# Optimization experiments

Hardware: AMD Instinct MI355X
Metric: run time of the kernel (lower is better)

The kernel has to match this reference:

```python
import jax, jax.numpy as jnp
import numpy as np

B, C, H, W = 4, 96, 56, 56
K0, K1, DIL, HID = 5, 7, 3, 4  # HID: ConvMlp(dim, expansion, drop) => hidden_features = int(mlp_ratio) = 4 (repo quirk)
EPS = 1e-5


def _conv(x, w, b, pad, dil=1, groups=1):
    y = jax.lax.conv_general_dilated(x, w, (1, 1), [(pad, pad), (pad, pad)],
                                     rhs_dilation=(dil, dil),
                                     dimension_numbers=('NCHW', 'OIHW', 'NCHW'),
                                     feature_group_count=groups)
    return y + b[None, :, None, None]


def _conv1x1(x, w, b):
    return jnp.einsum('bchw,oc->bohw', x, w) + b[None, :, None, None]


def _ln(x, g, b):
    # LayerNormProxy: LayerNorm over channel dim of NCHW
    mu = jnp.mean(x, axis=1, keepdims=True)
    v = jnp.var(x, axis=1, keepdims=True)
    return (x - mu) * jax.lax.rsqrt(v + EPS) * g[None, :, None, None] + b[None, :, None, None]


def _gelu(x):
    return jax.nn.gelu(x, approximate=False)  # torch nn.GELU default = exact erf


def _deform_dw(x, ow, ob, dw, db, k, dil, pad):
    # DeformConv2d wrapper: offsets from a same-geometry conv, then depthwise deformable conv.
    Bx, Cx, Hx, Wx = x.shape
    P = k * k
    off = _conv(x, ow, ob, pad, dil).reshape(Bx, P, 2, Hx, Wx)  # [B,P,(y,x),H,W]
    ky = (jnp.repeat(jnp.arange(k), k) * dil - pad).astype(x.dtype)  # row-major kernel grid
    kx = (jnp.tile(jnp.arange(k), k) * dil - pad).astype(x.dtype)
    py = jnp.arange(Hx, dtype=x.dtype)[None, None, :, None] + ky[None, :, None, None] + off[:, :, 0]
    px = jnp.arange(Wx, dtype=x.dtype)[None, None, None, :] + kx[None, :, None, None] + off[:, :, 1]
    y0 = jnp.floor(py)
    x0 = jnp.floor(px)
    wy = py - y0
    wx = px - x0
    xf = x.reshape(Bx, Cx, Hx * Wx)

    def corner(yi, xi):
        valid = (yi >= 0) & (yi < Hx) & (xi >= 0) & (xi < Wx)
        idx = (jnp.clip(yi, 0, Hx - 1).astype(jnp.int32) * Wx
               + jnp.clip(xi, 0, Wx - 1).astype(jnp.int32)).reshape(Bx, -1)
        g = jax.vmap(lambda a, i: jnp.take(a, i, axis=1))(xf, idx).reshape(Bx, Cx, P, Hx, Wx)
        return g * valid[:, None].astype(x.dtype)

    v = (corner(y0, x0) * ((1 - wy) * (1 - wx))[:, None]
         + corner(y0, x0 + 1) * ((1 - wy) * wx)[:, None]
         + corner(y0 + 1, x0) * (wy * (1 - wx))[:, None]
         + corner(y0 + 1, x0 + 1) * (wy * wx)[:, None])  # [B,C,P,H,W]
    return jnp.einsum('bcphw,cp->bchw', v, dw) + db[None, :, None, None]


def setup_inputs() -> dict:
    key = jax.random.key(0)
    ks = iter(jax.random.split(key, 32))

    def rn(shape, s=1.0):
        return jax.random.normal(next(ks), shape, jnp.float32) * s

    f32 = jnp.float32
    return {
        'x': rn((B, C, H, W)),
        'g1n': jnp.ones((C,), f32), 'b1n': jnp.zeros((C,), f32),
        'p1w': rn((C, C), 1 / np.sqrt(C)), 'p1b': jnp.zeros((C,), f32),
        'o0w': rn((2 * K0 * K0, C, K0, K0), 0.05 / np.sqrt(C * K0 * K0)), 'o0b': jnp.zeros((2 * K0 * K0,), f32),
        'd0w': rn((C, K0 * K0), 1 / np.sqrt(K0 * K0)), 'd0b': jnp.zeros((C,), f32),
        'o1w': rn((2 * K1 * K1, C, K1, K1), 0.05 / np.sqrt(C * K1 * K1)), 'o1b': jnp.zeros((2 * K1 * K1,), f32),
        'd1w': rn((C, K1 * K1), 1 / np.sqrt(K1 * K1)), 'd1b': jnp.zeros((C,), f32),
        'c1w': rn((C, C), 1 / np.sqrt(C)), 'c1b': jnp.zeros((C,), f32),
        'p2w': rn((C, C), 1 / np.sqrt(C)), 'p2b': jnp.zeros((C,), f32),
        'ls1': jnp.full((C,), 0.01, f32),
        'g2n': jnp.ones((C,), f32), 'b2n': jnp.zeros((C,), f32),
        'f1w': rn((HID, C), 1 / np.sqrt(C)), 'f1b': jnp.zeros((HID,), f32),
        'dww': rn((HID, 1, 3, 3), 1 / 3.0), 'dwb': jnp.zeros((HID,), f32),
        'f2w': rn((C, HID), 1 / np.sqrt(HID)), 'f2b': jnp.zeros((C,), f32),
        'ls2': jnp.full((C,), 0.01, f32),
    }


def reference(x, g1n, b1n, p1w, p1b, o0w, o0b, d0w, d0b, o1w, o1b, d1w, d1b,
              c1w, c1b, p2w, p2b, ls1, g2n, b2n, f1w, f1b, dww, dwb, f2w, f2b, ls2):
    # attention branch
    y = _ln(x, g1n, b1n)
    shortcut = y
    y = _gelu(_conv1x1(y, p1w, p1b))
    u = y
    a = _deform_dw(y, o0w, o0b, d0w, d0b, K0, 1, K0 // 2)
    a = _deform_dw(a, o1w, o1b, d1w, d1b, K1, DIL, (K1 // 2) * DIL)
    a = _conv1x1(a, c1w, c1b)
    y = _conv1x1(u * a, p2w, p2b) + shortcut
    y = ls1[None, :, None, None] * y
    x = x + y
    # MLP branch (note: norm2 is applied to the branch output y, as in the source)
    z = _ln(y, g2n, b2n)
    z = _conv1x1(z, f1w, f1b)
    z = _gelu(_conv(z, dww, dwb, 1, 1, HID))
    z = _conv1x1(z, f2w, f2b)
    x = x + ls2[None, :, None, None] * z
    return x
```

## Files before the change

### kernel.cpp

```cpp
#include <hip/hip_runtime.h>
#include <math.h>

namespace {

constexpr int Bc = 4, Cc = 96, Hc = 56, Wc = 56;
constexpr int HWc = Hc * Wc;
constexpr int Nc  = Bc * HWc;
constexpr float EPSc = 1e-5f;

typedef __attribute__((ext_vector_type(8))) short bf16x8;
typedef __attribute__((ext_vector_type(4))) float f32x4;

__device__ __forceinline__ unsigned short f2bf(float f) {
  union { float f; unsigned u; } x; x.f = f;
  unsigned r = x.u + 0x7fffu + ((x.u >> 16) & 1u);
  return (unsigned short)(r >> 16);
}
__device__ __forceinline__ float bf2f(unsigned short u) {
  union { unsigned u; float f; } x; x.u = (unsigned)u << 16; return x.f;
}
__device__ __forceinline__ float gelu_exact(float x) {
  return 0.5f * x * (1.0f + erff(x * 0.7071067811865475f));
}

__global__ __launch_bounds__(256) void k_ln(const float* __restrict__ x,
                                            const float* __restrict__ g,
                                            const float* __restrict__ b,
                                            unsigned short* __restrict__ outN) {
  int pos = blockIdx.x * 256 + threadIdx.x;
  int bb = pos / HWc, hw = pos % HWc;
  const float* xb = x + (size_t)bb * Cc * HWc + hw;
  float s = 0.f, s2 = 0.f;
  for (int c = 0; c < Cc; ++c) { float v = xb[c * HWc]; s += v; s2 += v * v; }
  float mu  = s * (1.f / Cc);
  float var = fmaxf(s2 * (1.f / Cc) - mu * mu, 0.f);
  float rs  = rsqrtf(var + EPSc);
  unsigned short* ob = outN + (size_t)pos * Cc;
  for (int q = 0; q < 12; ++q) {
    unsigned short t8[8];
#pragma unroll
    for (int j = 0; j < 8; ++j) {
      int c = q * 8 + j;
      t8[j] = f2bf((xb[c * HWc] - mu) * rs * g[c] + b[c]);
    }
    *reinterpret_cast<bf16x8*>(ob + q * 8) = *reinterpret_cast<const bf16x8*>(t8);
  }
}

template <int K_, int MTILES, int P>
__global__ __launch_bounds__(256) void k_pack_w(const float* __restrict__ wsrc,
                                                unsigned short* __restrict__ wpk) {
  constexpr int TOTAL = K_ * K_ * 3 * MTILES * 512;
  int idx = blockIdx.x * 256 + threadIdx.x;
  if (idx >= TOTAL) return;
  int j    = idx & 7;
  int lane = (idx >> 3) & 63;
  int t    = idx >> 9;
  int mt   = t % MTILES;
  int step = t / MTILES;
  int o = mt * 16 + (lane & 15);
  int k = step * 32 + ((lane >> 4) & 3) * 8 + j;
  int p = k / Cc, c = k % Cc;
  float v = 0.f;
  if (o < P) v = wsrc[(((size_t)o * Cc + c) * K_ + p / K_) * K_ + (p % K_)];
  wpk[idx] = f2bf(v);
}

__global__ __launch_bounds__(256) void k_pack_dwt(const float* __restrict__ dwsrc,
                                                  float* __restrict__ dwt, int KK) {
  int idx = blockIdx.x * 256 + threadIdx.x;
  if (idx >= KK * Cc) return;
  int p = idx / Cc, c = idx % Cc;
  dwt[idx] = dwsrc[c * KK + p];
}

template <int GELU, int PADP, int WP>
__global__ __launch_bounds__(256) void k_pwg(const unsigned short* __restrict__ inN,
                                             const unsigned short* __restrict__ wpk,
                                             const float* __restrict__ bq,
                                             unsigned short* __restrict__ outPad) {
  int lane = threadIdx.x & 63;
  int wv = threadIdx.x >> 6;
  int ng = wv & 1, mg = wv >> 1;
  int n = blockIdx.x * 32 + ng * 16 + (lane & 15);
  int ko = ((lane >> 4) & 3) * 8;
  const unsigned short* ib = inN + (size_t)n * Cc + ko;
  const unsigned short* wl = wpk + (size_t)lane * 8;
  f32x4 acc[3];
#pragma unroll
  for (int m = 0; m < 3; ++m) acc[m] = (f32x4){0.f, 0.f, 0.f, 0.f};
#pragma unroll
  for (int ks = 0; ks < 3; ++ks) {
    bf16x8 bf = *reinterpret_cast<const bf16x8*>(ib + ks * 32);
#pragma unroll
    for (int m = 0; m < 3; ++m) {
      bf16x8 af = *reinterpret_cast<const bf16x8*>(wl + (size_t)(ks * 6 + mg * 3 + m) * 512);
      acc[m] = __builtin_amdgcn_mfma_f32_16x16x32_bf16(af, bf, acc[m], 0, 0, 0);
    }
  }
  int bb = n / HWc, hw = n % HWc;
  int h = hw / Wc, w = hw % Wc;
  unsigned short* ob = outPad + (((size_t)bb * (Hc + 2 * PADP) + h + PADP) * WP + w + PADP) * Cc;
  int orow = ((lane >> 4) & 3) * 4;
#pragma unroll
  for (int m = 0; m < 3; ++m) {
    int o0 = (mg * 3 + m) * 16 + orow;
    float4 bv = *reinterpret_cast<const float4*>(bq + o0);
    unsigned short t4[4];
#pragma unroll
    for (int j = 0; j < 4; ++j) {
      float r = acc[m][j] + ((const float*)&bv)[j];
      if (GELU) r = gelu_exact(r);
      t4[j] = f2bf(r);
    }
    *reinterpret_cast<uint2*>(ob + o0) = *reinterpret_cast<const uint2*>(t4);
  }
}

template <int UPADP, int UWP>
__global__ __launch_bounds__(256) void k_comb(const unsigned short* __restrict__ uPad,
                                              const unsigned short* __restrict__ An,
                                              const unsigned short* __restrict__ wpk,
                                              const float* __restrict__ bq,
                                              const unsigned short* __restrict__ ylnN,
                                              const float* __restrict__ ls1q,
                                              const float* __restrict__ x,
                                              float* __restrict__ out,
                                              unsigned short* __restrict__ y2N) {
  int lane = threadIdx.x & 63;
  int wv = threadIdx.x >> 6;
  int ng = wv & 1, mg = wv >> 1;
  int n = blockIdx.x * 32 + ng * 16 + (lane & 15);
  int ko = ((lane >> 4) & 3) * 8;
  int bb = n / HWc, hw = n % HWc;
  int h = hw / Wc, w = hw % Wc;
  const unsigned short* ub = uPad + (((size_t)bb * (Hc + 2 * UPADP) + h + UPADP) * UWP + w + UPADP) * Cc + ko;
  const unsigned short* ab = An + (size_t)n * Cc + ko;
  const unsigned short* wl = wpk + (size_t)lane * 8;
  f32x4 acc[3];
#pragma unroll
  for (int m = 0; m < 3; ++m) acc[m] = (f32x4){0.f, 0.f, 0.f, 0.f};
#pragma unroll
  for (int ks = 0; ks < 3; ++ks) {
    bf16x8 uv = *reinterpret_cast<const bf16x8*>(ub + ks * 32);
    bf16x8 av = *reinterpret_cast<const bf16x8*>(ab + ks * 32);
    union { bf16x8 v; unsigned short s[8]; } uu, aa, gg;
    uu.v = uv; aa.v = av;
#pragma unroll
    for (int j = 0; j < 8; ++j) gg.s[j] = f2bf(bf2f(uu.s[j]) * bf2f(aa.s[j]));
#pragma unroll
    for (int m = 0; m < 3; ++m) {
      bf16x8 af = *reinterpret_cast<const bf16x8*>(wl + (size_t)(ks * 6 + mg * 3 + m) * 512);
      acc[m] = __builtin_amdgcn_mfma_f32_16x16x32_bf16(af, gg.v, acc[m], 0, 0, 0);
    }
  }
  int orow = ((lane >> 4) & 3) * 4;
  const float* xb = x + (size_t)bb * Cc * HWc + hw;
  float* ob = out + (size_t)bb * Cc * HWc + hw;
#pragma unroll
  for (int m = 0; m < 3; ++m) {
    int o0 = (mg * 3 + m) * 16 + orow;
    float4 bv = *reinterpret_cast<const float4*>(bq + o0);
    float4 lv = *reinterpret_cast<const float4*>(ls1q + o0);
    uint2 yl = *reinterpret_cast<const uint2*>(ylnN + (size_t)n * Cc + o0);
    unsigned short yl4[4];
    *reinterpret_cast<uint2*>(yl4) = yl;
    unsigned short t4[4];
#pragma unroll
    for (int j = 0; j < 4; ++j) {
      float t = acc[m][j] + ((const float*)&bv)[j] + bf2f(yl4[j]);
      float y2 = ((const float*)&lv)[j] * t;
      t4[j] = f2bf(y2);
      ob[(size_t)(o0 + j) * HWc] = xb[(size_t)(o0 + j) * HWc] + y2;
    }
    *reinterpret_cast<uint2*>(y2N + (size_t)n * Cc + o0) = *reinterpret_cast<const uint2*>(t4);
  }
}

template <int K_, int DIL_, int MTILES, int MT, int P, int PADP, int WP, int PSTR>
__global__ __launch_bounds__(256) void k_conv_mfma(const unsigned short* __restrict__ inp,
                                                   const unsigned short* __restrict__ wpk,
                                                   const float* __restrict__ bq,
                                                   float* __restrict__ dstT) {
  constexpr int KK = K_ * K_;
  constexpr int HP = Hc + 2 * PADP;
  constexpr int NBLK = Nc / 32;
  int lane = threadIdx.x & 63;
  int wv = threadIdx.x >> 6;
  int bid = blockIdx.x;
  int ntile = (bid & 7) * (NBLK / 8) + (bid >> 3);
  int n0 = ntile * 32 + (lane & 15);
  int n1 = n0 + 16;
  int b0 = n0 / HWc, hw0 = n0 % HWc, h0 = hw0 / Wc, w0 = hw0 % Wc;
  int b1 = n1 / HWc, hw1 = n1 % HWc, h1 = hw1 / Wc, w1 = hw1 % Wc;
  int co = ((lane >> 4) & 3) * 8;
  const unsigned short* ib0 = inp + ((size_t)b0 * HP * WP + (size_t)h0 * WP + w0) * Cc + co;
  const unsigned short* ib1 = inp + ((size_t)b1 * HP * WP + (size_t)h1 * WP + w1) * Cc + co;
  const unsigned short* wl = wpk + (size_t)lane * 8;
  int mt0 = wv * MT;
  int mtc[MT];
#pragma unroll
  for (int i = 0; i < MT; ++i) mtc[i] = min(mt0 + i, MTILES - 1);

  f32x4 acc[MT][2];
#pragma unroll
  for (int i = 0; i < MT; ++i) {
    acc[i][0] = (f32x4){0.f, 0.f, 0.f, 0.f};
    acc[i][1] = (f32x4){0.f, 0.f, 0.f, 0.f};
  }

  bf16x8 Bb[3][2], Aa[MT][3];
#pragma unroll
  for (int cc = 0; cc < 3; ++cc) {
    Bb[cc][0] = *reinterpret_cast<const bf16x8*>(ib0 + cc * 32);
    Bb[cc][1] = *reinterpret_cast<const bf16x8*>(ib1 + cc * 32);
#pragma unroll
    for (int i = 0; i < MT; ++i)
      Aa[i][cc] = *reinterpret_cast<const bf16x8*>(wl + ((size_t)cc * MTILES + mtc[i]) * 512);
  }

#pragma unroll 2
  for (int p = 0; p < KK; ++p) {
    int pn = (p + 1 < KK) ? p + 1 : p;
    size_t toff = (size_t)((pn / K_) * DIL_ * WP + (pn % K_) * DIL_) * Cc;
    const unsigned short* sp0 = ib0 + toff;
    const unsigned short* sp1 = ib1 + toff;
    bf16x8 Bn[3][2], An[MT][3];
#pragma unroll
    for (int cc = 0; cc < 3; ++cc) {
      Bn[cc][0] = *reinterpret_cast<const bf16x8*>(sp0 + cc * 32);
      Bn[cc][1] = *reinterpret_cast<const bf16x8*>(sp1 + cc * 32);
#pragma unroll
      for (int i = 0; i < MT; ++i)
        An[i][cc] = *reinterpret_cast<const bf16x8*>(wl + ((size_t)(pn * 3 + cc) * MTILES + mtc[i]) * 512);
    }
#pragma unroll
    for (int cc = 0; cc < 3; ++cc)
#pragma unroll
      for (int i = 0; i < MT; ++i) {
        acc[i][0] = __builtin_amdgcn_mfma_f32_16x16x32_bf16(Aa[i][cc], Bb[cc][0], acc[i][0], 0, 0, 0);
        acc[i][1] = __builtin_amdgcn_mfma_f32_16x16x32_bf16(Aa[i][cc], Bb[cc][1], acc[i][1], 0, 0, 0);
      }
#pragma unroll
    for (int cc = 0; cc < 3; ++cc) {
      Bb[cc][0] = Bn[cc][0];
      Bb[cc][1] = Bn[cc][1];
#pragma unroll
      for (int i = 0; i < MT; ++i) Aa[i][cc] = An[i][cc];
    }
  }

  int orow = ((lane >> 4) & 3) * 4;
#pragma unroll
  for (int i = 0; i < MT; ++i) {
    int mt = mt0 + i;
    if (mt >= MTILES) break;
#pragma unroll
    for (int nt = 0; nt < 2; ++nt) {
      float4 st;
#pragma unroll
      for (int j = 0; j < 4; ++j) {
        int o = mt * 16 + orow + j;
        float bias = (o < P) ? bq[o] : 0.f;
        ((float*)&st)[j] = acc[i][nt][j] + bias;
      }
      int n = nt ? n1 : n0;
      *reinterpret_cast<float4*>(dstT + (size_t)n * PSTR + mt * 16 + orow) = st;
    }
  }
}

template <int K_, int DIL_, int PAD_, int IPADP, int IWP, int OPADP, int OWP, int PSTR>
__global__ __launch_bounds__(256) void k_deform(const unsigned short* __restrict__ srcT,
                                                const float* __restrict__ offT,
                                                const float* __restrict__ dwt,
                                                const float* __restrict__ dbq,
                                                float* __restrict__ dst,
                                                unsigned short* __restrict__ dstPad) {
  constexpr int KK = K_ * K_;
  constexpr int KK4 = KK & ~3;
  constexpr int IHP = Hc + 2 * IPADP;
  int tid = blockIdx.x * 256 + threadIdx.x;
  int cg = tid % 24;
  int pos = tid / 24;
  int c = cg * 4;
  int bb = pos / HWc, hw = pos % HWc;
  int h = hw / Wc, w = hw % Wc;
  const unsigned short* sb = srcT + (size_t)bb * IHP * IWP * Cc + c;
  const float* ob = offT + (size_t)pos * PSTR;
  float ax = 0.f, ay = 0.f, az = 0.f, aw = 0.f;

  for (int pg = 0; pg < KK4; pg += 4) {
    float4 o01 = *reinterpret_cast<const float4*>(ob + 2 * pg);
    float4 o23 = *reinterpret_cast<const float4*>(ob + 2 * pg + 4);
    float oyv[4] = {o01.x, o01.z, o23.x, o23.z};
    float oxv[4] = {o01.y, o01.w, o23.y, o23.w};
    uint2 v[4][4];
    float wt[4][4];
#pragma unroll
    for (int i = 0; i < 4; ++i) {
      int p = pg + i;
      float py = (float)(h + (p / K_) * DIL_ - PAD_) + oyv[i];
      float px = (float)(w + (p % K_) * DIL_ - PAD_) + oxv[i];
      float y0f = floorf(py), x0f = floorf(px);
      float wy = py - y0f, wx = px - x0f;
      int y0 = (int)y0f, x0 = (int)x0f;
#pragma unroll
      for (int dy = 0; dy < 2; ++dy) {
        int yi = y0 + dy;
        bool yv = (unsigned)yi < (unsigned)Hc;
        int yc = min(max(yi, 0), Hc - 1);
        float wyv = dy ? wy : 1.f - wy;
#pragma unroll
        for (int dx = 0; dx < 2; ++dx) {
          int xi = x0 + dx;
          bool xv = (unsigned)xi < (unsigned)Wc;
          int xc = min(max(xi, 0), Wc - 1);
          wt[i][dy * 2 + dx] = (yv && xv) ? wyv * (dx ? wx : 1.f - wx) : 0.f;
          v[i][dy * 2 + dx] = *reinterpret_cast<const uint2*>(
              sb + ((size_t)(yc + IPADP) * IWP + (xc + IPADP)) * Cc);
        }
      }
    }
#pragma unroll
    for (int i = 0; i < 4; ++i) {
      int p = pg + i;
      float4 d = *reinterpret_cast<const float4*>(dwt + (size_t)p * Cc + c);
      float sx = 0.f, sy = 0.f, sz = 0.f, sw = 0.f;
#pragma unroll
      for (int q = 0; q < 4; ++q) {
        float wq_ = wt[i][q];
        sx += wq_ * bf2f((unsigned short)(v[i][q].x & 0xffffu));
        sy += wq_ * bf2f((unsigned short)(v[i][q].x >> 16));
        sz += wq_ * bf2f((unsigned short)(v[i][q].y & 0xffffu));
        sw += wq_ * bf2f((unsigned short)(v[i][q].y >> 16));
      }
      ax += sx * d.x; ay += sy * d.y; az += sz * d.z; aw += sw * d.w;
    }
  }
  {
    int p = KK - 1;
    float oy = ob[2 * p], ox = ob[2 * p + 1];
    float py = (float)(h + (p / K_) * DIL_ - PAD_) + oy;
    float px = (float)(w + (p % K_) * DIL_ - PAD_) + ox;
    float y0f = floorf(py), x0f = floorf(px);
    float wy = py - y0f, wx = px - x0f;
    int y0 = (int)y0f, x0 = (int)x0f;
    uint2 v[4]; float wt[4];
#pragma unroll
    for (int dy = 0; dy < 2; ++dy) {
      int yi = y0 + dy;
      bool yv = (unsigned)yi < (unsigned)Hc;
      int yc = min(max(yi, 0), Hc - 1);
      float wyv = dy ? wy : 1.f - wy;
#pragma unroll
      for (int dx = 0; dx < 2; ++dx) {
        int xi = x0 + dx;
        bool xv = (unsigned)xi < (unsigned)Wc;
        int xc = min(max(xi, 0), Wc - 1);
        wt[dy * 2 + dx] = (yv && xv) ? wyv * (dx ? wx : 1.f - wx) : 0.f;
        v[dy * 2 + dx] = *reinterpret_cast<const uint2*>(
            sb + ((size_t)(yc + IPADP) * IWP + (xc + IPADP)) * Cc);
      }
    }
    float4 d = *reinterpret_cast<const float4*>(dwt + (size_t)p * Cc + c);
    float sx = 0.f, sy = 0.f, sz = 0.f, sw = 0.f;
#pragma unroll
    for (int q = 0; q < 4; ++q) {
      sx += wt[q] * bf2f((unsigned short)(v[q].x & 0xffffu));
      sy += wt[q] * bf2f((unsigned short)(v[q].x >> 16));
      sz += wt[q] * bf2f((unsigned short)(v[q].y & 0xffffu));
      sw += wt[q] * bf2f((unsigned short)(v[q].y >> 16));
    }
    ax += sx * d.x; ay += sy * d.y; az += sz * d.z; aw += sw * d.w;
  }

  ax += dbq[c]; ay += dbq[c + 1]; az += dbq[c + 2]; aw += dbq[c + 3];
  if (dst) {
    float* d = dst + (size_t)bb * Cc * HWc + hw;
    d[(c + 0) * HWc] = ax; d[(c + 1) * HWc] = ay;
    d[(c + 2) * HWc] = az; d[(c + 3) * HWc] = aw;
  }
  if (dstPad) {
    unsigned short t4[4] = {f2bf(ax), f2bf(ay), f2bf(az), f2bf(aw)};
    unsigned short* tb = dstPad + (((size_t)bb * (Hc + 2 * OPADP) + h + OPADP) * OWP + w + OPADP) * Cc + c;
    *reinterpret_cast<uint2*>(tb) = *reinterpret_cast<const uint2*>(t4);
  }
}

__global__ __launch_bounds__(256) void k_mlp1(const unsigned short* __restrict__ y2N,
                                              const float* __restrict__ g,
                                              const float* __restrict__ b,
                                              const float* __restrict__ f1wq,
                                              const float* __restrict__ f1bq,
                                              float* __restrict__ z4) {
  int pos = blockIdx.x * 256 + threadIdx.x;
  int bb = pos / HWc, hw = pos % HWc;
  const unsigned short* yb = y2N + (size_t)pos * Cc;
  float vv[96];
  float s = 0.f, s2 = 0.f;
#pragma unroll
  for (int q = 0; q < 12; ++q) {
    bf16x8 t = *reinterpret_cast<const bf16x8*>(yb + q * 8);
    union { bf16x8 v; unsigned short s[8]; } u; u.v = t;
#pragma unroll
    for (int j = 0; j < 8; ++j) {
      float f = bf2f(u.s[j]);
      vv[q * 8 + j] = f; s += f; s2 += f * f;
    }
  }
  float mu  = s * (1.f / Cc);
  float var = fmaxf(s2 * (1.f / Cc) - mu * mu, 0.f);
  float rs  = rsqrtf(var + EPSc);
  float a0 = 0.f, a1 = 0.f, a2 = 0.f, a3 = 0.f;
#pragma unroll
  for (int c = 0; c < 96; ++c) {
    float t = (vv[c] - mu) * rs * g[c] + b[c];
    a0 += t * f1wq[0 * Cc + c];
    a1 += t * f1wq[1 * Cc + c];
    a2 += t * f1wq[2 * Cc + c];
    a3 += t * f1wq[3 * Cc + c];
  }
  float* zb = z4 + (size_t)bb * 4 * HWc + hw;
  zb[0 * HWc] = a0 + f1bq[0];
  zb[1 * HWc] = a1 + f1bq[1];
  zb[2 * HWc] = a2 + f1bq[2];
  zb[3 * HWc] = a3 + f1bq[3];
}

__global__ __launch_bounds__(256) void k_mlp_dw(const float* __restrict__ z4,
                                                const float* __restrict__ dwwq,
                                                const float* __restrict__ dwbq,
                                                float* __restrict__ z4b) {
  int tid = blockIdx.x * 256 + threadIdx.x;
  int hw = tid % HWc;
  int bj = tid / HWc;
  int j = bj % 4;
  int h = hw / Wc, w = hw % Wc;
  const float* zb = z4 + (size_t)bj * HWc;
  float s = 0.f;
#pragma unroll
  for (int ky = 0; ky < 3; ++ky) {
    int y = h + ky - 1;
    if ((unsigned)y >= (unsigned)Hc) continue;
#pragma unroll
    for (int kx = 0; kx < 3; ++kx) {
      int x = w + kx - 1;
      if ((unsigned)x >= (unsigned)Wc) continue;
      s += zb[y * Wc + x] * dwwq[j * 9 + ky * 3 + kx];
    }
  }
  z4b[tid] = gelu_exact(s + dwbq[j]);
}

__global__ __launch_bounds__(256) void k_mlp2(const float* __restrict__ z4b,
                                              const float* __restrict__ f2wq,
                                              const float* __restrict__ f2bq,
                                              const float* __restrict__ ls2q,
                                              float* __restrict__ out) {
  int pos = blockIdx.x * 256 + threadIdx.x;
  int bb = pos / HWc, hw = pos % HWc;
  const float* zb = z4b + (size_t)bb * 4 * HWc + hw;
  float z0 = zb[0 * HWc], z1 = zb[1 * HWc], z2 = zb[2 * HWc], z3 = zb[3 * HWc];
  float* ob = out + (size_t)bb * Cc * HWc + hw;
  for (int o = 0; o < Cc; ++o) {
    float s = f2bq[o] + z0 * f2wq[o * 4 + 0] + z1 * f2wq[o * 4 + 1]
                      + z2 * f2wq[o * 4 + 2] + z3 * f2wq[o * 4 + 3];
    ob[o * HWc] += ls2q[o] * s;
  }
}

}

extern "C" void kernel_launch(void* const* d_in, const int* in_sizes, int n_in,
                              void* d_out, int out_size, void* d_ws, size_t ws_size,
                              hipStream_t stream) {
  (void)in_sizes; (void)n_in; (void)out_size; (void)ws_size;
  const float* x   = (const float*)d_in[0];
  const float* g1n = (const float*)d_in[1];
  const float* b1n = (const float*)d_in[2];
  const float* p1w = (const float*)d_in[3];
  const float* p1b = (const float*)d_in[4];
  const float* o0w = (const float*)d_in[5];
  const float* o0b = (const float*)d_in[6];
  const float* d0w = (const float*)d_in[7];
  const float* d0b = (const float*)d_in[8];
  const float* o1w = (const float*)d_in[9];
  const float* o1b = (const float*)d_in[10];
  const float* d1w = (const float*)d_in[11];
  const float* d1b = (const float*)d_in[12];
  const float* c1w = (const float*)d_in[13];
  const float* c1b = (const float*)d_in[14];
  const float* p2w = (const float*)d_in[15];
  const float* p2b = (const float*)d_in[16];
  const float* ls1 = (const float*)d_in[17];
  const float* g2n = (const float*)d_in[18];
  const float* b2n = (const float*)d_in[19];
  const float* f1w = (const float*)d_in[20];
  const float* f1b = (const float*)d_in[21];
  const float* dww = (const float*)d_in[22];
  const float* dwb = (const float*)d_in[23];
  const float* f2w = (const float*)d_in[24];
  const float* f2b = (const float*)d_in[25];
  const float* ls2 = (const float*)d_in[26];
  float* out = (float*)d_out;
  float* ws  = (float*)d_ws;

  float* off0t = ws;                                  size_t o_ = (size_t)Nc * 64;
  float* off1t = ws + o_;                             o_ += (size_t)Nc * 112;
  float* z4    = ws + o_;                             o_ += (size_t)Bc * 4 * HWc;
  float* z4b   = ws + o_;                             o_ += (size_t)Bc * 4 * HWc;
  float* dwt0  = ws + o_;                             o_ += 25 * Cc;
  float* dwt1  = ws + o_;                             o_ += 49 * Cc;
  unsigned short* yln_n  = (unsigned short*)(ws + o_); o_ += (size_t)Nc * Cc / 2;
  unsigned short* a1_n   = (unsigned short*)(ws + o_); o_ += (size_t)Nc * Cc / 2;
  unsigned short* A_n    = (unsigned short*)(ws + o_); o_ += (size_t)Nc * Cc / 2;
  unsigned short* y2_n   = (unsigned short*)(ws + o_); o_ += (size_t)Nc * Cc / 2;
  unsigned short* u_pad  = (unsigned short*)(ws + o_); o_ += (size_t)Bc * 60 * 60 * Cc / 2;
  unsigned short* a0_pad = (unsigned short*)(ws + o_); o_ += (size_t)Bc * 74 * 74 * Cc / 2;
  unsigned short* wpk0   = (unsigned short*)(ws + o_); o_ += (size_t)25 * 3 * 4 * 512 / 2;
  unsigned short* wpk1   = (unsigned short*)(ws + o_); o_ += (size_t)49 * 3 * 7 * 512 / 2;
  unsigned short* wpkp1  = (unsigned short*)(ws + o_); o_ += (size_t)3 * 6 * 512 / 2;
  unsigned short* wpkc1  = (unsigned short*)(ws + o_); o_ += (size_t)3 * 6 * 512 / 2;
  unsigned short* wpkp2  = (unsigned short*)(ws + o_); o_ += (size_t)3 * 6 * 512 / 2;

  dim3 b256(256, 1, 1);

  hipMemsetAsync(u_pad, 0, (size_t)Bc * 60 * 60 * Cc * sizeof(unsigned short), stream);
  hipMemsetAsync(a0_pad, 0, (size_t)Bc * 74 * 74 * Cc * sizeof(unsigned short), stream);
  hipLaunchKernelGGL((k_pack_w<5, 4, 50>), dim3((25 * 3 * 4 * 512 + 255) / 256), b256, 0, stream, o0w, wpk0);
  hipLaunchKernelGGL((k_pack_w<7, 7, 98>), dim3((49 * 3 * 7 * 512 + 255) / 256), b256, 0, stream, o1w, wpk1);
  hipLaunchKernelGGL((k_pack_w<1, 6, 96>), dim3((3 * 6 * 512 + 255) / 256), b256, 0, stream, p1w, wpkp1);
  hipLaunchKernelGGL((k_pack_w<1, 6, 96>), dim3((3 * 6 * 512 + 255) / 256), b256, 0, stream, c1w, wpkc1);
  hipLaunchKernelGGL((k_pack_w<1, 6, 96>), dim3((3 * 6 * 512 + 255) / 256), b256, 0, stream, p2w, wpkp2);
  hipLaunchKernelGGL(k_pack_dwt, dim3((25 * Cc + 255) / 256), b256, 0, stream, d0w, dwt0, 25);
  hipLaunchKernelGGL(k_pack_dwt, dim3((49 * Cc + 255) / 256), b256, 0, stream, d1w, dwt1, 49);

  hipLaunchKernelGGL(k_ln, dim3(Nc / 256), b256, 0, stream, x, g1n, b1n, yln_n);
  hipLaunchKernelGGL((k_pwg<1, 2, 60>), dim3(Nc / 32), b256, 0, stream, yln_n, wpkp1, p1b, u_pad);
  hipLaunchKernelGGL((k_conv_mfma<5, 1, 4, 1, 50, 2, 60, 64>), dim3(Nc / 32), b256, 0, stream,
                     u_pad, wpk0, o0b, off0t);
  hipLaunchKernelGGL((k_deform<5, 1, 2, 2, 60, 9, 74, 64>), dim3(Nc * 24 / 256), b256, 0, stream,
                     u_pad, off0t, dwt0, d0b, (float*)nullptr, a0_pad);
  hipLaunchKernelGGL((k_conv_mfma<7, 3, 7, 2, 98, 9, 74, 112>), dim3(Nc / 32), b256, 0, stream,
                     a0_pad, wpk1, o1b, off1t);
  hipLaunchKernelGGL((k_deform<7, 3, 9, 9, 74, 0, 56, 112>), dim3(Nc * 24 / 256), b256, 0, stream,
                     a0_pad, off1t, dwt1, d1b, (float*)nullptr, a1_n);
  hipLaunchKernelGGL((k_pwg<0, 0, 56>), dim3(Nc / 32), b256, 0, stream, a1_n, wpkc1, c1b, A_n);
  hipLaunchKernelGGL((k_comb<2, 60>), dim3(Nc / 32), b256, 0, stream,
                     u_pad, A_n, wpkp2, p2b, yln_n, ls1, x, out, y2_n);
  hipLaunchKernelGGL(k_mlp1, dim3(Nc / 256), b256, 0, stream, y2_n, g2n, b2n, f1w, f1b, z4);
  hipLaunchKernelGGL(k_mlp_dw, dim3(Nc * 4 / 256), b256, 0, stream, z4, dww, dwb, z4b);
  hipLaunchKernelGGL(k_mlp2, dim3(Nc / 256), b256, 0, stream, z4b, f2w, f2b, ls2, out);
}
```

Measured before the change: 223.6 us.

## Split offset-conv MFMA work across 8 waves, one 16-column half per wave

The implicit-GEMM offset convolution kernel now uses 512-thread blocks. Each wave handles one 16-pixel half of the 32-pixel tile for its group of output M-tiles, instead of one wave covering both halves. The tap loop is rewritten as an explicit two-stage ping-pong (load tap p+2 while computing tap p+1). The aim is more waves per block to hide global-load latency and a lower per-wave register count from halved accumulators and input buffers. The cost is that each weight fragment is now loaded by two waves, doubling weight traffic.

Result: slower. 243.1 us (+8.7%).

```diff
diff --git a/kernel.cpp b/kernel.cpp
--- a/kernel.cpp
+++ b/kernel.cpp
@@ -178,7 +178,7 @@
 }
 
 template <int K_, int DIL_, int MTILES, int MT, int P, int PADP, int WP, int PSTR>
-__global__ __launch_bounds__(256) void k_conv_mfma(const unsigned short* __restrict__ inp,
+__global__ __launch_bounds__(512) void k_conv_mfma(const unsigned short* __restrict__ inp,
                                                    const unsigned short* __restrict__ wpk,
                                                    const float* __restrict__ bq,
                                                    float* __restrict__ dstT) {
@@ -187,86 +187,72 @@
   constexpr int NBLK = Nc / 32;
   int lane = threadIdx.x & 63;
   int wv = threadIdx.x >> 6;
+  int nh = wv & 1, mg = wv >> 1;
   int bid = blockIdx.x;
   int ntile = (bid & 7) * (NBLK / 8) + (bid >> 3);
-  int n0 = ntile * 32 + (lane & 15);
-  int n1 = n0 + 16;
-  int b0 = n0 / HWc, hw0 = n0 % HWc, h0 = hw0 / Wc, w0 = hw0 % Wc;
-  int b1 = n1 / HWc, hw1 = n1 % HWc, h1 = hw1 / Wc, w1 = hw1 % Wc;
+  int n = ntile * 32 + nh * 16 + (lane & 15);
+  int b = n / HWc, hw = n % HWc;
+  int h = hw / Wc, w = hw % Wc;
   int co = ((lane >> 4) & 3) * 8;
-  const unsigned short* ib0 = inp + ((size_t)b0 * HP * WP + (size_t)h0 * WP + w0) * Cc + co;
-  const unsigned short* ib1 = inp + ((size_t)b1 * HP * WP + (size_t)h1 * WP + w1) * Cc + co;
+  const unsigned short* ib = inp + ((size_t)b * HP * WP + (size_t)h * WP + w) * Cc + co;
   const unsigned short* wl = wpk + (size_t)lane * 8;
-  int mt0 = wv * MT;
   int mtc[MT];
 #pragma unroll
-  for (int i = 0; i < MT; ++i) mtc[i] = min(mt0 + i, MTILES - 1);
-
-  f32x4 acc[MT][2];
+  for (int i = 0; i < MT; ++i) mtc[i] = min(mg * MT + i, MTILES - 1);
+
+  f32x4 acc[MT];
+#pragma unroll
+  for (int i = 0; i < MT; ++i) acc[i] = (f32x4){0.f, 0.f, 0.f, 0.f};
+
+  bf16x8 B0[3], A0[MT][3], B1[3], A1[MT][3];
+
+#define LOAD_TAP(Bb, Ab, pp)                                                          \
+  {                                                                                   \
+    size_t toff_ = (size_t)(((pp) / K_) * DIL_ * WP + ((pp) % K_) * DIL_) * Cc;       \
+    _Pragma("unroll")                                                                 \
+    for (int cc = 0; cc < 3; ++cc) {                                                  \
+      Bb[cc] = *reinterpret_cast<const bf16x8*>(ib + toff_ + cc * 32);                \
+      _Pragma("unroll")                                                               \
+      for (int i = 0; i < MT; ++i)                                                    \
+        Ab[i][cc] = *reinterpret_cast<const bf16x8*>(                                 \
+            wl + ((size_t)((pp) * 3 + cc) * MTILES + mtc[i]) * 512);                  \
+    }                                                                                 \
+  }
+#define MFMA_TAP(Bb, Ab)                                                              \
+  {                                                                                   \
+    _Pragma("unroll")                                                                 \
+    for (int cc = 0; cc < 3; ++cc)                                                    \
+      _Pragma("unroll")                                                               \
+      for (int i = 0; i < MT; ++i)                                                    \
+        acc[i] = __builtin_amdgcn_mfma_f32_16x16x32_bf16(Ab[i][cc], Bb[cc], acc[i],   \
+                                                         0, 0, 0);                    \
+  }
+
+  LOAD_TAP(B0, A0, 0)
+  LOAD_TAP(B1, A1, 1)
+  for (int p = 0; p + 2 < KK; p += 2) {
+    MFMA_TAP(B0, A0)
+    LOAD_TAP(B0, A0, p + 2)
+    MFMA_TAP(B1, A1)
+    if (p + 3 < KK) LOAD_TAP(B1, A1, p + 3)
+  }
+  MFMA_TAP(B0, A0)
+#undef LOAD_TAP
+#undef MFMA_TAP
+
+  int orow = ((lane >> 4) & 3) * 4;
 #pragma unroll
   for (int i = 0; i < MT; ++i) {
-    acc[i][0] = (f32x4){0.f, 0.f, 0.f, 0.f};
-    acc[i][1] = (f32x4){0.f, 0.f, 0.f, 0.f};
-  }
-
-  bf16x8 Bb[3][2], Aa[MT][3];
-#pragma unroll
-  for (int cc = 0; cc < 3; ++cc) {
-    Bb[cc][0] = *reinterpret_cast<const bf16x8*>(ib0 + cc * 32);
-    Bb[cc][1] = *reinterpret_cast<const bf16x8*>(ib1 + cc * 32);
-#pragma unroll
-    for (int i = 0; i < MT; ++i)
-      Aa[i][cc] = *reinterpret_cast<const bf16x8*>(wl + ((size_t)cc * MTILES + mtc[i]) * 512);
-  }
-
-#pragma unroll 2
-  for (int p = 0; p < KK; ++p) {
-    int pn = (p + 1 < KK) ? p + 1 : p;
-    size_t toff = (size_t)((pn / K_) * DIL_ * WP + (pn % K_) * DIL_) * Cc;
-    const unsigned short* sp0 = ib0 + toff;
-    const unsigned short* sp1 = ib1 + toff;
-    bf16x8 Bn[3][2], An[MT][3];
-#pragma unroll
-    for (int cc = 0; cc < 3; ++cc) {
-      Bn[cc][0] = *reinterpret_cast<const bf16x8*>(sp0 + cc * 32);
-      Bn[cc][1] = *reinterpret_cast<const bf16x8*>(sp1 + cc * 32);
-#pragma unroll
-      for (int i = 0; i < MT; ++i)
-        An[i][cc] = *reinterpret_cast<const bf16x8*>(wl + ((size_t)(pn * 3 + cc) * MTILES + mtc[i]) * 512);
-    }
-#pragma unroll
-    for (int cc = 0; cc < 3; ++cc)
-#pragma unroll
-      for (int i = 0; i < MT; ++i) {
-        acc[i][0] = __builtin_amdgcn_mfma_f32_16x16x32_bf16(Aa[i][cc], Bb[cc][0], acc[i][0], 0, 0, 0);
-        acc[i][1] = __builtin_amdgcn_mfma_f32_16x16x32_bf16(Aa[i][cc], Bb[cc][1], acc[i][1], 0, 0, 0);
-      }
-#pragma unroll
-    for (int cc = 0; cc < 3; ++cc) {
-      Bb[cc][0] = Bn[cc][0];
-      Bb[cc][1] = Bn[cc][1];
-#pragma unroll
-      for (int i = 0; i < MT; ++i) Aa[i][cc] = An[i][cc];
-    }
-  }
-
-  int orow = ((lane >> 4) & 3) * 4;
-#pragma unroll
-  for (int i = 0; i < MT; ++i) {
-    int mt = mt0 + i;
+    int mt = mg * MT + i;
     if (mt >= MTILES) break;
-#pragma unroll
-    for (int nt = 0; nt < 2; ++nt) {
-      float4 st;
-#pragma unroll
-      for (int j = 0; j < 4; ++j) {
-        int o = mt * 16 + orow + j;
-        float bias = (o < P) ? bq[o] : 0.f;
-        ((float*)&st)[j] = acc[i][nt][j] + bias;
-      }
-      int n = nt ? n1 : n0;
-      *reinterpret_cast<float4*>(dstT + (size_t)n * PSTR + mt * 16 + orow) = st;
-    }
+    float4 st;
+#pragma unroll
+    for (int j = 0; j < 4; ++j) {
+      int o = mt * 16 + orow + j;
+      float bias = (o < P) ? bq[o] : 0.f;
+      ((float*)&st)[j] = acc[i][j] + bias;
+    }
+    *reinterpret_cast<float4*>(dstT + (size_t)n * PSTR + mt * 16 + orow) = st;
   }
 }
 
@@ -524,7 +510,7 @@
   unsigned short* wpkc1  = (unsigned short*)(ws + o_); o_ += (size_t)3 * 6 * 512 / 2;
   unsigned short* wpkp2  = (unsigned short*)(ws + o_); o_ += (size_t)3 * 6 * 512 / 2;
 
-  dim3 b256(256, 1, 1);
+  dim3 b256(256, 1, 1), b512(512, 1, 1);
 
   hipMemsetAsync(u_pad, 0, (size_t)Bc * 60 * 60 * Cc * sizeof(unsigned short), stream);
   hipMemsetAsync(a0_pad, 0, (size_t)Bc * 74 * 74 * Cc * sizeof(unsigned short), stream);
@@ -538,11 +524,11 @@
 
   hipLaunchKernelGGL(k_ln, dim3(Nc / 256), b256, 0, stream, x, g1n, b1n, yln_n);
   hipLaunchKernelGGL((k_pwg<1, 2, 60>), dim3(Nc / 32), b256, 0, stream, yln_n, wpkp1, p1b, u_pad);
-  hipLaunchKernelGGL((k_conv_mfma<5, 1, 4, 1, 50, 2, 60, 64>), dim3(Nc / 32), b256, 0, stream,
+  hipLaunchKernelGGL((k_conv_mfma<5, 1, 4, 1, 50, 2, 60, 64>), dim3(Nc / 32), b512, 0, stream,
                      u_pad, wpk0, o0b, off0t);
   hipLaunchKernelGGL((k_deform<5, 1, 2, 2, 60, 9, 74, 64>), dim3(Nc * 24 / 256), b256, 0, stream,
                      u_pad, off0t, dwt0, d0b, (float*)nullptr, a0_pad);
-  hipLaunchKernelGGL((k_conv_mfma<7, 3, 7, 2, 98, 9, 74, 112>), dim3(Nc / 32), b256, 0, stream,
+  hipLaunchKernelGGL((k_conv_mfma<7, 3, 7, 2, 98, 9, 74, 112>), dim3(Nc / 32), b512, 0, stream,
                      a0_pad, wpk1, o1b, off1t);
   hipLaunchKernelGGL((k_deform<7, 3, 9, 9, 74, 0, 56, 112>), dim3(Nc * 24 / 256), b256, 0, stream,
                      a0_pad, off1t, dwt1, d1b, (float*)nullptr, a1_n);
```

## Split offset-conv kernel taps across grid y and sum partials in deform

Applied to the files above, without the earlier changes.

The offset-producing MFMA convolutions now split their kernel-tap loop across blockIdx.y (2 splits for the 5x5 conv, 4 for the 7x7 dilated conv). Each split writes its partial sums to a separate buffer, and the deform kernels add the partial offsets as they load them. Bias is applied only in the first split. This gives the long serial tap loop more parallelism and more waves in flight, at the cost of extra partial-offset writes and reads and a larger workspace.

Measured after the change: 233.8 us. 4.6% more time.

```diff
diff --git a/kernel.cpp b/kernel.cpp
--- a/kernel.cpp
+++ b/kernel.cpp
@@ -177,17 +177,21 @@
   }
 }
 
-template <int K_, int DIL_, int MTILES, int MT, int P, int PADP, int WP, int PSTR>
+template <int K_, int DIL_, int MTILES, int MT, int P, int PADP, int WP, int PSTR, int SPLIT>
 __global__ __launch_bounds__(256) void k_conv_mfma(const unsigned short* __restrict__ inp,
                                                    const unsigned short* __restrict__ wpk,
                                                    const float* __restrict__ bq,
                                                    float* __restrict__ dstT) {
   constexpr int KK = K_ * K_;
+  constexpr int KKbase = KK / SPLIT, KKrem = KK % SPLIT;
   constexpr int HP = Hc + 2 * PADP;
   constexpr int NBLK = Nc / 32;
   int lane = threadIdx.x & 63;
   int wv = threadIdx.x >> 6;
   int bid = blockIdx.x;
+  int sp = blockIdx.y;
+  int p0 = sp * KKbase + min(sp, KKrem);
+  int pcnt = KKbase + (sp < KKrem ? 1 : 0);
   int ntile = (bid & 7) * (NBLK / 8) + (bid >> 3);
   int n0 = ntile * 32 + (lane & 15);
   int n1 = n0 + 16;
@@ -210,18 +214,21 @@
   }
 
   bf16x8 Bb[3][2], Aa[MT][3];
-#pragma unroll
-  for (int cc = 0; cc < 3; ++cc) {
-    Bb[cc][0] = *reinterpret_cast<const bf16x8*>(ib0 + cc * 32);
-    Bb[cc][1] = *reinterpret_cast<const bf16x8*>(ib1 + cc * 32);
-#pragma unroll
-    for (int i = 0; i < MT; ++i)
-      Aa[i][cc] = *reinterpret_cast<const bf16x8*>(wl + ((size_t)cc * MTILES + mtc[i]) * 512);
+  {
+    size_t toff = (size_t)((p0 / K_) * DIL_ * WP + (p0 % K_) * DIL_) * Cc;
+#pragma unroll
+    for (int cc = 0; cc < 3; ++cc) {
+      Bb[cc][0] = *reinterpret_cast<const bf16x8*>(ib0 + toff + cc * 32);
+      Bb[cc][1] = *reinterpret_cast<const bf16x8*>(ib1 + toff + cc * 32);
+#pragma unroll
+      for (int i = 0; i < MT; ++i)
+        Aa[i][cc] = *reinterpret_cast<const bf16x8*>(wl + ((size_t)(p0 * 3 + cc) * MTILES + mtc[i]) * 512);
+    }
   }
 
 #pragma unroll 2
-  for (int p = 0; p < KK; ++p) {
-    int pn = (p + 1 < KK) ? p + 1 : p;
+  for (int pi = 0; pi < pcnt; ++pi) {
+    int pn = p0 + ((pi + 1 < pcnt) ? pi + 1 : pi);
     size_t toff = (size_t)((pn / K_) * DIL_ * WP + (pn % K_) * DIL_) * Cc;
     const unsigned short* sp0 = ib0 + toff;
     const unsigned short* sp1 = ib1 + toff;
@@ -250,6 +257,7 @@
     }
   }
 
+  float* dsp = dstT + (size_t)sp * Nc * PSTR;
   int orow = ((lane >> 4) & 3) * 4;
 #pragma unroll
   for (int i = 0; i < MT; ++i) {
@@ -261,16 +269,16 @@
 #pragma unroll
       for (int j = 0; j < 4; ++j) {
         int o = mt * 16 + orow + j;
-        float bias = (o < P) ? bq[o] : 0.f;
+        float bias = (sp == 0 && o < P) ? bq[o] : 0.f;
         ((float*)&st)[j] = acc[i][nt][j] + bias;
       }
       int n = nt ? n1 : n0;
-      *reinterpret_cast<float4*>(dstT + (size_t)n * PSTR + mt * 16 + orow) = st;
-    }
-  }
-}
-
-template <int K_, int DIL_, int PAD_, int IPADP, int IWP, int OPADP, int OWP, int PSTR>
+      *reinterpret_cast<float4*>(dsp + (size_t)n * PSTR + mt * 16 + orow) = st;
+    }
+  }
+}
+
+template <int K_, int DIL_, int PAD_, int IPADP, int IWP, int OPADP, int OWP, int PSTR, int NSUM>
 __global__ __launch_bounds__(256) void k_deform(const unsigned short* __restrict__ srcT,
                                                 const float* __restrict__ offT,
                                                 const float* __restrict__ dwt,
@@ -293,6 +301,14 @@
   for (int pg = 0; pg < KK4; pg += 4) {
     float4 o01 = *reinterpret_cast<const float4*>(ob + 2 * pg);
     float4 o23 = *reinterpret_cast<const float4*>(ob + 2 * pg + 4);
+#pragma unroll
+    for (int q = 1; q < NSUM; ++q) {
+      const float* obq = ob + (size_t)q * Nc * PSTR;
+      float4 a01 = *reinterpret_cast<const float4*>(obq + 2 * pg);
+      float4 a23 = *reinterpret_cast<const float4*>(obq + 2 * pg + 4);
+      o01.x += a01.x; o01.y += a01.y; o01.z += a01.z; o01.w += a01.w;
+      o23.x += a23.x; o23.y += a23.y; o23.z += a23.z; o23.w += a23.w;
+    }
     float oyv[4] = {o01.x, o01.z, o23.x, o23.z};
     float oxv[4] = {o01.y, o01.w, o23.y, o23.w};
     uint2 v[4][4];
@@ -341,6 +357,11 @@
   {
     int p = KK - 1;
     float oy = ob[2 * p], ox = ob[2 * p + 1];
+#pragma unroll
+    for (int q = 1; q < NSUM; ++q) {
+      const float* obq = ob + (size_t)q * Nc * PSTR;
+      oy += obq[2 * p]; ox += obq[2 * p + 1];
+    }
     float py = (float)(h + (p / K_) * DIL_ - PAD_) + oy;
     float px = (float)(w + (p % K_) * DIL_ - PAD_) + ox;
     float y0f = floorf(py), x0f = floorf(px);
@@ -506,8 +527,8 @@
   float* out = (float*)d_out;
   float* ws  = (float*)d_ws;
 
-  float* off0t = ws;                                  size_t o_ = (size_t)Nc * 64;
-  float* off1t = ws + o_;                             o_ += (size_t)Nc * 112;
+  float* off0t = ws;                                  size_t o_ = (size_t)2 * Nc * 64;
+  float* off1t = ws + o_;                             o_ += (size_t)4 * Nc * 112;
   float* z4    = ws + o_;                             o_ += (size_t)Bc * 4 * HWc;
   float* z4b   = ws + o_;                             o_ += (size_t)Bc * 4 * HWc;
   float* dwt0  = ws + o_;                             o_ += 25 * Cc;
@@ -538,13 +559,13 @@
 
   hipLaunchKernelGGL(k_ln, dim3(Nc / 256), b256, 0, stream, x, g1n, b1n, yln_n);
   hipLaunchKernelGGL((k_pwg<1, 2, 60>), dim3(Nc / 32), b256, 0, stream, yln_n, wpkp1, p1b, u_pad);
-  hipLaunchKernelGGL((k_conv_mfma<5, 1, 4, 1, 50, 2, 60, 64>), dim3(Nc / 32), b256, 0, stream,
+  hipLaunchKernelGGL((k_conv_mfma<5, 1, 4, 1, 50, 2, 60, 64, 2>), dim3(Nc / 32, 2), b256, 0, stream,
                      u_pad, wpk0, o0b, off0t);
-  hipLaunchKernelGGL((k_deform<5, 1, 2, 2, 60, 9, 74, 64>), dim3(Nc * 24 / 256), b256, 0, stream,
+  hipLaunchKernelGGL((k_deform<5, 1, 2, 2, 60, 9, 74, 64, 2>), dim3(Nc * 24 / 256), b256, 0, stream,
                      u_pad, off0t, dwt0, d0b, (float*)nullptr, a0_pad);
-  hipLaunchKernelGGL((k_conv_mfma<7, 3, 7, 2, 98, 9, 74, 112>), dim3(Nc / 32), b256, 0, stream,
+  hipLaunchKernelGGL((k_conv_mfma<7, 3, 7, 2, 98, 9, 74, 112, 4>), dim3(Nc / 32, 4), b256, 0, stream,
                      a0_pad, wpk1, o1b, off1t);
-  hipLaunchKernelGGL((k_deform<7, 3, 9, 9, 74, 0, 56, 112>), dim3(Nc * 24 / 256), b256, 0, stream,
+  hipLaunchKernelGGL((k_deform<7, 3, 9, 9, 74, 0, 56, 112, 4>), dim3(Nc * 24 / 256), b256, 0, stream,
                      a0_pad, off1t, dwt1, d1b, (float*)nullptr, a1_n);
   hipLaunchKernelGGL((k_pwg<0, 0, 56>), dim3(Nc / 32), b256, 0, stream, a1_n, wpkc1, c1b, A_n);
   hipLaunchKernelGGL((k_comb<2, 60>), dim3(Nc / 32), b256, 0, stream,
```
